# Kernel tuning notes

Measured on AMD Instinct MI355X. Metric: run time of the kernel, lower is better.

Reference implementation:

```python
import jax, jax.numpy as jnp
import numpy as np

B, S, FEAT, DK = 128, 2048, 512, 64

def setup_inputs() -> dict:
    key = jax.random.key(0)
    k1, k2, k3, k4, k5 = jax.random.split(key, 5)
    input_k = jax.random.normal(k1, (B, S, FEAT), dtype=jnp.float32)
    input_q = jax.random.normal(k2, (B, FEAT), dtype=jnp.float32)
    context_len = jax.random.randint(k3, (B,), 0, S + 1, dtype=jnp.int32)
    # Linear weights stored as [in, out] so y = x @ W
    W_K = jax.random.normal(k4, (FEAT, DK), dtype=jnp.float32) / np.sqrt(FEAT)
    W_Q = jax.random.normal(k5, (FEAT, DK), dtype=jnp.float32) / np.sqrt(FEAT)
    return {"input_k": input_k, "input_q": input_q, "context_len": context_len,
            "W_K": W_K, "W_Q": W_Q}

def reference(input_k, input_q, context_len, W_K, W_Q):
    # K: [B,S,dk], q: [B,dk]
    K = jnp.einsum('bsf,fd->bsd', input_k, W_K)
    q = input_q @ W_Q
    scores = jnp.einsum('bd,bsd->bs', q, K)  # [B,S] (n_heads=1, no scaling in original)
    mask = jnp.arange(S)[None, :] < context_len[:, None]  # [B,S]
    attn = jax.nn.softmax(jnp.where(mask, scores, -1e30), axis=-1)  # [B,S]
    context = jnp.einsum('bs,bsf->bf', attn, input_k)  # [B,FEAT]
    # length==0 rows produce zeros in the original
    context = jnp.where((context_len > 0)[:, None], context, 0.0)
    return context
```

## Files before the change

kernel.cpp:

```cpp
#include <hip/hip_runtime.h>
#include <math.h>

#define B_    128
#define S_    2048
#define FEAT_ 512
#define DK_   64
#define NSPLIT 16

typedef float f32x4 __attribute__((ext_vector_type(4)));

__device__ __forceinline__ float dot8(f32x4 x0, f32x4 x1, f32x4 v0, f32x4 v1) {
  float p = x0[0] * v0[0];
  p = fmaf(x0[1], v0[1], p);
  p = fmaf(x0[2], v0[2], p);
  p = fmaf(x0[3], v0[3], p);
  p = fmaf(x1[0], v1[0], p);
  p = fmaf(x1[1], v1[1], p);
  p = fmaf(x1[2], v1[2], p);
  p = fmaf(x1[3], v1[3], p);
  return p;
}

__device__ __forceinline__ float wredsum(float p) {
#pragma unroll
  for (int off = 32; off; off >>= 1) p += __shfl_xor(p, off, 64);
  return p;
}

__global__ __launch_bounds__(256) void qv_kernel(
    const float* __restrict__ input_q, const float* __restrict__ W_Q,
    const float* __restrict__ W_K, float* __restrict__ v) {
  int b = blockIdx.x;
  int tid = threadIdx.x;
  __shared__ float xq[FEAT_];
  __shared__ float part[4][DK_];
  __shared__ float qs[DK_];
  for (int f = tid; f < FEAT_; f += 256) xq[f] = input_q[b * FEAT_ + f];
  __syncthreads();
  {
    int d = tid & 63, c = tid >> 6;
    float s = 0.f;
    int f0 = c * 128;
    for (int f = f0; f < f0 + 128; ++f) s = fmaf(xq[f], W_Q[f * DK_ + d], s);
    part[c][d] = s;
  }
  __syncthreads();
  if (tid < DK_)
    qs[tid] = part[0][tid] + part[1][tid] + part[2][tid] + part[3][tid];
  __syncthreads();
  for (int f = tid; f < FEAT_; f += 256) {
    const f32x4* wk = (const f32x4*)(W_K + f * DK_);
    float s = 0.f;
#pragma unroll
    for (int d4 = 0; d4 < DK_ / 4; ++d4) {
      f32x4 w = wk[d4];
      s = fmaf(w[0], qs[d4 * 4 + 0], s);
      s = fmaf(w[1], qs[d4 * 4 + 1], s);
      s = fmaf(w[2], qs[d4 * 4 + 2], s);
      s = fmaf(w[3], qs[d4 * 4 + 3], s);
    }
    v[b * FEAT_ + f] = s;
  }
}

__global__ __launch_bounds__(256) void pass_kernel(
    const float* __restrict__ input_k, const int* __restrict__ ctx,
    const float* __restrict__ v, float* __restrict__ pm,
    float* __restrict__ pl, float* __restrict__ pacc) {
  int b = blockIdx.x;
  int split = blockIdx.y;
  int L = ctx[b];
  int tid = threadIdx.x, wave = tid >> 6, lane = tid & 63;
  int idx = b * NSPLIT + split;

  int s0 = (split * L) / NSPLIT;
  int s1 = ((split + 1) * L) / NSPLIT;

  if (s0 >= s1) {
    if (tid == 0) { pm[idx] = -INFINITY; pl[idx] = 0.f; }
    return;
  }

  const float* vb = v + b * FEAT_ + lane * 4;
  f32x4 v0 = *(const f32x4*)vb;
  f32x4 v1 = *(const f32x4*)(vb + 256);

  float m = -INFINITY, l = 0.f;
  f32x4 a0 = {0.f, 0.f, 0.f, 0.f};
  f32x4 a1 = {0.f, 0.f, 0.f, 0.f};

  const float* base = input_k + (size_t)b * S_ * FEAT_;
  int s = s0 + wave;

  for (; s + 12 < s1; s += 16) {
    const float* r_ = base + (size_t)s * FEAT_ + lane * 4;
    f32x4 x0 = *(const f32x4*)(r_);
    f32x4 x1 = *(const f32x4*)(r_ + 256);
    f32x4 x2 = *(const f32x4*)(r_ + 4 * FEAT_);
    f32x4 x3 = *(const f32x4*)(r_ + 4 * FEAT_ + 256);
    f32x4 x4 = *(const f32x4*)(r_ + 8 * FEAT_);
    f32x4 x5 = *(const f32x4*)(r_ + 8 * FEAT_ + 256);
    f32x4 x6 = *(const f32x4*)(r_ + 12 * FEAT_);
    f32x4 x7 = *(const f32x4*)(r_ + 12 * FEAT_ + 256);

    float p0 = dot8(x0, x1, v0, v1);
    float p1 = dot8(x2, x3, v0, v1);
    float p2 = dot8(x4, x5, v0, v1);
    float p3 = dot8(x6, x7, v0, v1);
    p0 = wredsum(p0);
    p1 = wredsum(p1);
    p2 = wredsum(p2);
    p3 = wredsum(p3);
    float mn = fmaxf(fmaxf(fmaxf(p0, p1), fmaxf(p2, p3)), m);
    float sc = __expf(m - mn);
    float w0 = __expf(p0 - mn), w1 = __expf(p1 - mn);
    float w2 = __expf(p2 - mn), w3 = __expf(p3 - mn);
    l = fmaf(l, sc, (w0 + w1) + (w2 + w3));
#pragma unroll
    for (int j = 0; j < 4; ++j) {
      a0[j] = fmaf(w0, x0[j],
              fmaf(w1, x2[j], fmaf(w2, x4[j], fmaf(w3, x6[j], a0[j] * sc))));
      a1[j] = fmaf(w0, x1[j],
              fmaf(w1, x3[j], fmaf(w2, x5[j], fmaf(w3, x7[j], a1[j] * sc))));
    }
    m = mn;
  }
  for (; s < s1; s += 4) {
    const float* r_ = base + (size_t)s * FEAT_ + lane * 4;
    f32x4 x0 = *(const f32x4*)(r_);
    f32x4 x1 = *(const f32x4*)(r_ + 256);
    float p = wredsum(dot8(x0, x1, v0, v1));
    float mn = fmaxf(m, p);
    float sc = __expf(m - mn);
    float w = __expf(p - mn);
    l = fmaf(l, sc, w);
#pragma unroll
    for (int j = 0; j < 4; ++j) {
      a0[j] = fmaf(w, x0[j], a0[j] * sc);
      a1[j] = fmaf(w, x1[j], a1[j] * sc);
    }
    m = mn;
  }

  __shared__ float sm[4], sl[4];
  __shared__ float sa[4][FEAT_];
  if (lane == 0) { sm[wave] = m; sl[wave] = l; }
  *(f32x4*)&sa[wave][lane * 4] = a0;
  *(f32x4*)&sa[wave][256 + lane * 4] = a1;
  __syncthreads();

  float M = fmaxf(fmaxf(sm[0], sm[1]), fmaxf(sm[2], sm[3]));
  float e0 = __expf(sm[0] - M), e1 = __expf(sm[1] - M);
  float e2 = __expf(sm[2] - M), e3 = __expf(sm[3] - M);
  if (tid == 0) {
    pm[idx] = M;
    pl[idx] = e0 * sl[0] + e1 * sl[1] + e2 * sl[2] + e3 * sl[3];
  }
  for (int f = tid; f < FEAT_; f += 256)
    pacc[(size_t)idx * FEAT_ + f] =
        e0 * sa[0][f] + e1 * sa[1][f] + e2 * sa[2][f] + e3 * sa[3][f];
}

__global__ __launch_bounds__(256) void combine_kernel(
    const float* __restrict__ pm, const float* __restrict__ pl,
    const float* __restrict__ pacc, float* __restrict__ out) {
  int b = blockIdx.x;
  int tid = threadIdx.x;
  __shared__ float e[NSPLIT];
  __shared__ float inv_s;
  if (tid < NSPLIT) {
    float mi = pm[b * NSPLIT + tid];
    float M = mi;
#pragma unroll
    for (int off = 8; off; off >>= 1) M = fmaxf(M, __shfl_xor(M, off, 64));
    float ei = (M == -INFINITY) ? 0.f : __expf(mi - M);
    e[tid] = ei;
    float lw = ei * pl[b * NSPLIT + tid];
#pragma unroll
    for (int off = 8; off; off >>= 1) lw += __shfl_xor(lw, off, 64);
    if (tid == 0) inv_s = (lw > 0.f) ? 1.f / lw : 0.f;
  }
  __syncthreads();
  float inv = inv_s;
  for (int f = tid; f < FEAT_; f += 256) {
    float s = 0.f;
    for (int i = 0; i < NSPLIT; ++i)
      if (e[i] > 0.f)
        s = fmaf(e[i], pacc[((size_t)(b * NSPLIT + i)) * FEAT_ + f], s);
    out[b * FEAT_ + f] = s * inv;
  }
}

extern "C" void kernel_launch(void* const* d_in, const int* in_sizes, int n_in,
                              void* d_out, int out_size, void* d_ws, size_t ws_size,
                              hipStream_t stream) {
  const float* input_k = (const float*)d_in[0];
  const float* input_q = (const float*)d_in[1];
  const int*   ctx     = (const int*)d_in[2];
  const float* W_K     = (const float*)d_in[3];
  const float* W_Q     = (const float*)d_in[4];
  float* out = (float*)d_out;

  char* ws = (char*)d_ws;
  float* v    = (float*)ws;
  float* pm   = (float*)(ws + (size_t)B_ * FEAT_ * sizeof(float));
  float* pl   = pm + B_ * NSPLIT;
  float* pacc = pl + B_ * NSPLIT;

  qv_kernel<<<B_, 256, 0, stream>>>(input_q, W_Q, W_K, v);
  pass_kernel<<<dim3(B_, NSPLIT), 256, 0, stream>>>(input_k, ctx, v, pm, pl, pacc);
  combine_kernel<<<B_, 256, 0, stream>>>(pm, pl, pacc, out);
}
```

Measured before the change: 71.87 us.

## Use persistent blocks with atomic work queue and finer sequence splits

Replaces the fixed (batch, split) grid with a persistent pool of blocks that take (batch, split) tasks from a global atomic counter. The counter is reset in the qv kernel. The number of splits per row doubles to 32, which shrinks the task size so uneven context lengths balance better across CUs. The cost is one atomic and two barriers per task, twice as many partial results for the combine kernel to reduce, and a dependence on kernel ordering for the counter reset.

```diff
diff --git a/kernel.cpp b/kernel.cpp
--- a/kernel.cpp
+++ b/kernel.cpp
@@ -5,7 +5,9 @@
 #define S_    2048
 #define FEAT_ 512
 #define DK_   64
-#define NSPLIT 16
+#define NSPLIT 32
+#define NTASKS (B_ * NSPLIT)
+#define NBLOCKS 2048
 
 typedef float f32x4 __attribute__((ext_vector_type(4)));
 
@@ -29,9 +31,11 @@
 
 __global__ __launch_bounds__(256) void qv_kernel(
     const float* __restrict__ input_q, const float* __restrict__ W_Q,
-    const float* __restrict__ W_K, float* __restrict__ v) {
+    const float* __restrict__ W_K, float* __restrict__ v,
+    unsigned* __restrict__ counter) {
   int b = blockIdx.x;
   int tid = threadIdx.x;
+  if (b == 0 && tid == 0) *counter = 0u;
   __shared__ float xq[FEAT_];
   __shared__ float part[4][DK_];
   __shared__ float qs[DK_];
@@ -66,99 +70,110 @@
 __global__ __launch_bounds__(256) void pass_kernel(
     const float* __restrict__ input_k, const int* __restrict__ ctx,
     const float* __restrict__ v, float* __restrict__ pm,
-    float* __restrict__ pl, float* __restrict__ pacc) {
-  int b = blockIdx.x;
-  int split = blockIdx.y;
-  int L = ctx[b];
+    float* __restrict__ pl, float* __restrict__ pacc,
+    unsigned* __restrict__ counter) {
   int tid = threadIdx.x, wave = tid >> 6, lane = tid & 63;
-  int idx = b * NSPLIT + split;
-
-  int s0 = (split * L) / NSPLIT;
-  int s1 = ((split + 1) * L) / NSPLIT;
-
-  if (s0 >= s1) {
-    if (tid == 0) { pm[idx] = -INFINITY; pl[idx] = 0.f; }
-    return;
-  }
-
-  const float* vb = v + b * FEAT_ + lane * 4;
-  f32x4 v0 = *(const f32x4*)vb;
-  f32x4 v1 = *(const f32x4*)(vb + 256);
-
-  float m = -INFINITY, l = 0.f;
-  f32x4 a0 = {0.f, 0.f, 0.f, 0.f};
-  f32x4 a1 = {0.f, 0.f, 0.f, 0.f};
-
-  const float* base = input_k + (size_t)b * S_ * FEAT_;
-  int s = s0 + wave;
-
-  for (; s + 12 < s1; s += 16) {
-    const float* r_ = base + (size_t)s * FEAT_ + lane * 4;
-    f32x4 x0 = *(const f32x4*)(r_);
-    f32x4 x1 = *(const f32x4*)(r_ + 256);
-    f32x4 x2 = *(const f32x4*)(r_ + 4 * FEAT_);
-    f32x4 x3 = *(const f32x4*)(r_ + 4 * FEAT_ + 256);
-    f32x4 x4 = *(const f32x4*)(r_ + 8 * FEAT_);
-    f32x4 x5 = *(const f32x4*)(r_ + 8 * FEAT_ + 256);
-    f32x4 x6 = *(const f32x4*)(r_ + 12 * FEAT_);
-    f32x4 x7 = *(const f32x4*)(r_ + 12 * FEAT_ + 256);
-
-    float p0 = dot8(x0, x1, v0, v1);
-    float p1 = dot8(x2, x3, v0, v1);
-    float p2 = dot8(x4, x5, v0, v1);
-    float p3 = dot8(x6, x7, v0, v1);
-    p0 = wredsum(p0);
-    p1 = wredsum(p1);
-    p2 = wredsum(p2);
-    p3 = wredsum(p3);
-    float mn = fmaxf(fmaxf(fmaxf(p0, p1), fmaxf(p2, p3)), m);
-    float sc = __expf(m - mn);
-    float w0 = __expf(p0 - mn), w1 = __expf(p1 - mn);
-    float w2 = __expf(p2 - mn), w3 = __expf(p3 - mn);
-    l = fmaf(l, sc, (w0 + w1) + (w2 + w3));
-#pragma unroll
-    for (int j = 0; j < 4; ++j) {
-      a0[j] = fmaf(w0, x0[j],
-              fmaf(w1, x2[j], fmaf(w2, x4[j], fmaf(w3, x6[j], a0[j] * sc))));
-      a1[j] = fmaf(w0, x1[j],
-              fmaf(w1, x3[j], fmaf(w2, x5[j], fmaf(w3, x7[j], a1[j] * sc))));
-    }
-    m = mn;
-  }
-  for (; s < s1; s += 4) {
-    const float* r_ = base + (size_t)s * FEAT_ + lane * 4;
-    f32x4 x0 = *(const f32x4*)(r_);
-    f32x4 x1 = *(const f32x4*)(r_ + 256);
-    float p = wredsum(dot8(x0, x1, v0, v1));
-    float mn = fmaxf(m, p);
-    float sc = __expf(m - mn);
-    float w = __expf(p - mn);
-    l = fmaf(l, sc, w);
-#pragma unroll
-    for (int j = 0; j < 4; ++j) {
-      a0[j] = fmaf(w, x0[j], a0[j] * sc);
-      a1[j] = fmaf(w, x1[j], a1[j] * sc);
-    }
-    m = mn;
-  }
-
   __shared__ float sm[4], sl[4];
   __shared__ float sa[4][FEAT_];
-  if (lane == 0) { sm[wave] = m; sl[wave] = l; }
-  *(f32x4*)&sa[wave][lane * 4] = a0;
-  *(f32x4*)&sa[wave][256 + lane * 4] = a1;
-  __syncthreads();
-
-  float M = fmaxf(fmaxf(sm[0], sm[1]), fmaxf(sm[2], sm[3]));
-  float e0 = __expf(sm[0] - M), e1 = __expf(sm[1] - M);
-  float e2 = __expf(sm[2] - M), e3 = __expf(sm[3] - M);
-  if (tid == 0) {
-    pm[idx] = M;
-    pl[idx] = e0 * sl[0] + e1 * sl[1] + e2 * sl[2] + e3 * sl[3];
-  }
-  for (int f = tid; f < FEAT_; f += 256)
-    pacc[(size_t)idx * FEAT_ + f] =
-        e0 * sa[0][f] + e1 * sa[1][f] + e2 * sa[2][f] + e3 * sa[3][f];
+  __shared__ unsigned s_task;
+
+  for (;;) {
+    if (tid == 0) s_task = atomicAdd(counter, 1u);
+    __syncthreads();
+    unsigned t = s_task;
+    __syncthreads();
+    if (t >= (unsigned)NTASKS) return;
+
+    int b = (int)(t >> 5);
+    int split = (int)(t & (NSPLIT - 1));
+    int L = ctx[b];
+    int idx = (int)t;
+
+    int s0 = (split * L) / NSPLIT;
+    int s1 = ((split + 1) * L) / NSPLIT;
+
+    if (s0 >= s1) {
+      if (tid == 0) { pm[idx] = -INFINITY; pl[idx] = 0.f; }
+      continue;
+    }
+
+    const float* vb = v + b * FEAT_ + lane * 4;
+    f32x4 v0 = *(const f32x4*)vb;
+    f32x4 v1 = *(const f32x4*)(vb + 256);
+
+    float m = -INFINITY, l = 0.f;
+    f32x4 a0 = {0.f, 0.f, 0.f, 0.f};
+    f32x4 a1 = {0.f, 0.f, 0.f, 0.f};
+
+    const float* base = input_k + (size_t)b * S_ * FEAT_;
+    int s = s0 + wave;
+
+    for (; s + 12 < s1; s += 16) {
+      const float* r_ = base + (size_t)s * FEAT_ + lane * 4;
+      f32x4 x0 = *(const f32x4*)(r_);
+      f32x4 x1 = *(const f32x4*)(r_ + 256);
+      f32x4 x2 = *(const f32x4*)(r_ + 4 * FEAT_);
+      f32x4 x3 = *(const f32x4*)(r_ + 4 * FEAT_ + 256);
+      f32x4 x4 = *(const f32x4*)(r_ + 8 * FEAT_);
+      f32x4 x5 = *(const f32x4*)(r_ + 8 * FEAT_ + 256);
+      f32x4 x6 = *(const f32x4*)(r_ + 12 * FEAT_);
+      f32x4 x7 = *(const f32x4*)(r_ + 12 * FEAT_ + 256);
+
+      float p0 = dot8(x0, x1, v0, v1);
+      float p1 = dot8(x2, x3, v0, v1);
+      float p2 = dot8(x4, x5, v0, v1);
+      float p3 = dot8(x6, x7, v0, v1);
+      p0 = wredsum(p0);
+      p1 = wredsum(p1);
+      p2 = wredsum(p2);
+      p3 = wredsum(p3);
+      float mn = fmaxf(fmaxf(fmaxf(p0, p1), fmaxf(p2, p3)), m);
+      float sc = __expf(m - mn);
+      float w0 = __expf(p0 - mn), w1 = __expf(p1 - mn);
+      float w2 = __expf(p2 - mn), w3 = __expf(p3 - mn);
+      l = fmaf(l, sc, (w0 + w1) + (w2 + w3));
+#pragma unroll
+      for (int j = 0; j < 4; ++j) {
+        a0[j] = fmaf(w0, x0[j],
+                fmaf(w1, x2[j], fmaf(w2, x4[j], fmaf(w3, x6[j], a0[j] * sc))));
+        a1[j] = fmaf(w0, x1[j],
+                fmaf(w1, x3[j], fmaf(w2, x5[j], fmaf(w3, x7[j], a1[j] * sc))));
+      }
+      m = mn;
+    }
+    for (; s < s1; s += 4) {
+      const float* r_ = base + (size_t)s * FEAT_ + lane * 4;
+      f32x4 x0 = *(const f32x4*)(r_);
+      f32x4 x1 = *(const f32x4*)(r_ + 256);
+      float p = wredsum(dot8(x0, x1, v0, v1));
+      float mn = fmaxf(m, p);
+      float sc = __expf(m - mn);
+      float w = __expf(p - mn);
+      l = fmaf(l, sc, w);
+#pragma unroll
+      for (int j = 0; j < 4; ++j) {
+        a0[j] = fmaf(w, x0[j], a0[j] * sc);
+        a1[j] = fmaf(w, x1[j], a1[j] * sc);
+      }
+      m = mn;
+    }
+
+    if (lane == 0) { sm[wave] = m; sl[wave] = l; }
+    *(f32x4*)&sa[wave][lane * 4] = a0;
+    *(f32x4*)&sa[wave][256 + lane * 4] = a1;
+    __syncthreads();
+
+    float M = fmaxf(fmaxf(sm[0], sm[1]), fmaxf(sm[2], sm[3]));
+    float e0 = __expf(sm[0] - M), e1 = __expf(sm[1] - M);
+    float e2 = __expf(sm[2] - M), e3 = __expf(sm[3] - M);
+    if (tid == 0) {
+      pm[idx] = M;
+      pl[idx] = e0 * sl[0] + e1 * sl[1] + e2 * sl[2] + e3 * sl[3];
+    }
+    for (int f = tid; f < FEAT_; f += 256)
+      pacc[(size_t)idx * FEAT_ + f] =
+          e0 * sa[0][f] + e1 * sa[1][f] + e2 * sa[2][f] + e3 * sa[3][f];
+  }
 }
 
 __global__ __launch_bounds__(256) void combine_kernel(
@@ -172,12 +187,12 @@
     float mi = pm[b * NSPLIT + tid];
     float M = mi;
 #pragma unroll
-    for (int off = 8; off; off >>= 1) M = fmaxf(M, __shfl_xor(M, off, 64));
+    for (int off = 16; off; off >>= 1) M = fmaxf(M, __shfl_xor(M, off, 64));
     float ei = (M == -INFINITY) ? 0.f : __expf(mi - M);
     e[tid] = ei;
     float lw = ei * pl[b * NSPLIT + tid];
 #pragma unroll
-    for (int off = 8; off; off >>= 1) lw += __shfl_xor(lw, off, 64);
+    for (int off = 16; off; off >>= 1) lw += __shfl_xor(lw, off, 64);
     if (tid == 0) inv_s = (lw > 0.f) ? 1.f / lw : 0.f;
   }
   __syncthreads();
@@ -204,10 +219,12 @@
   char* ws = (char*)d_ws;
   float* v    = (float*)ws;
   float* pm   = (float*)(ws + (size_t)B_ * FEAT_ * sizeof(float));
-  float* pl   = pm + B_ * NSPLIT;
-  float* pacc = pl + B_ * NSPLIT;
-
-  qv_kernel<<<B_, 256, 0, stream>>>(input_q, W_Q, W_K, v);
-  pass_kernel<<<dim3(B_, NSPLIT), 256, 0, stream>>>(input_k, ctx, v, pm, pl, pacc);
+  float* pl   = pm + NTASKS;
+  float* pacc = pl + NTASKS;
+  unsigned* counter = (unsigned*)(pacc + (size_t)NTASKS * FEAT_);
+
+  qv_kernel<<<B_, 256, 0, stream>>>(input_q, W_Q, W_K, v, counter);
+  pass_kernel<<<NBLOCKS, 256, 0, stream>>>(input_k, ctx, v, pm, pl, pacc,
+                                           counter);
   combine_kernel<<<B_, 256, 0, stream>>>(pm, pl, pacc, out);
 }
```

New measurement: 116.0 us. +61.3%, slower.

## Balance split-K attention work across blocks by context length

Applied to the files above, without the earlier changes.

Replaces the fixed 16 splits per batch row with a length-proportional allocation. About 1792 blocks are distributed across rows according to each row's context length, so every block handles a similar number of sequence positions. Each block works out its row and split index by scanning all 128 context lengths in a single thread, and the combine kernel recomputes the same prefix to find each row's partials. The aim is to remove the load imbalance that comes from random context lengths. The cost is a serial per-block scan and a combine step that can read up to 512 partials per row.

```diff
diff --git a/kernel.cpp b/kernel.cpp
--- a/kernel.cpp
+++ b/kernel.cpp
@@ -5,7 +5,9 @@
 #define S_    2048
 #define FEAT_ 512
 #define DK_   64
-#define NSPLIT 16
+#define NB    1792
+#define GRIDP 2048
+#define MAXN  512
 
 typedef float f32x4 __attribute__((ext_vector_type(4)));
 
@@ -27,6 +29,14 @@
   return p;
 }
 
+__device__ __forceinline__ int nsplits_of(int Lb, int T) {
+  if (T == 0) return 1;
+  int nb = (int)(((long long)Lb * NB + (T >> 1)) / T);
+  if (nb < 1) nb = 1;
+  if (nb > MAXN) nb = MAXN;
+  return nb;
+}
+
 __global__ __launch_bounds__(256) void qv_kernel(
     const float* __restrict__ input_q, const float* __restrict__ W_Q,
     const float* __restrict__ W_K, float* __restrict__ v) {
@@ -67,17 +77,39 @@
     const float* __restrict__ input_k, const int* __restrict__ ctx,
     const float* __restrict__ v, float* __restrict__ pm,
     float* __restrict__ pl, float* __restrict__ pacc) {
-  int b = blockIdx.x;
-  int split = blockIdx.y;
-  int L = ctx[b];
+  int j = blockIdx.x;
   int tid = threadIdx.x, wave = tid >> 6, lane = tid & 63;
-  int idx = b * NSPLIT + split;
-
-  int s0 = (split * L) / NSPLIT;
-  int s1 = ((split + 1) * L) / NSPLIT;
+
+  __shared__ int sL[B_];
+  __shared__ int sInfo[4];
+  __shared__ float sm[4], sl4[4];
+  __shared__ float sa[4][FEAT_];
+
+  if (tid < B_) sL[tid] = ctx[tid];
+  __syncthreads();
+  if (tid == 0) {
+    int T = 0;
+    for (int i = 0; i < B_; ++i) T += sL[i];
+    int q = 0, fb = -1, fk = 0, fL = 0, fn = 1;
+    for (int i = 0; i < B_; ++i) {
+      int nb = nsplits_of(sL[i], T);
+      if (fb < 0 && j >= q && j < q + nb) {
+        fb = i; fk = j - q; fL = sL[i]; fn = nb;
+      }
+      q += nb;
+    }
+    sInfo[0] = fb; sInfo[1] = fk; sInfo[2] = fL; sInfo[3] = fn;
+  }
+  __syncthreads();
+  int b = sInfo[0];
+  if (b < 0) return;
+  int k = sInfo[1], L = sInfo[2], nb = sInfo[3];
+
+  int s0 = (int)((long long)k * L / nb);
+  int s1 = (int)((long long)(k + 1) * L / nb);
 
   if (s0 >= s1) {
-    if (tid == 0) { pm[idx] = -INFINITY; pl[idx] = 0.f; }
+    if (tid == 0) { pm[j] = -INFINITY; pl[j] = 0.f; }
     return;
   }
 
@@ -117,11 +149,11 @@
     float w2 = __expf(p2 - mn), w3 = __expf(p3 - mn);
     l = fmaf(l, sc, (w0 + w1) + (w2 + w3));
 #pragma unroll
-    for (int j = 0; j < 4; ++j) {
-      a0[j] = fmaf(w0, x0[j],
-              fmaf(w1, x2[j], fmaf(w2, x4[j], fmaf(w3, x6[j], a0[j] * sc))));
-      a1[j] = fmaf(w0, x1[j],
-              fmaf(w1, x3[j], fmaf(w2, x5[j], fmaf(w3, x7[j], a1[j] * sc))));
+    for (int jj = 0; jj < 4; ++jj) {
+      a0[jj] = fmaf(w0, x0[jj],
+               fmaf(w1, x2[jj], fmaf(w2, x4[jj], fmaf(w3, x6[jj], a0[jj] * sc))));
+      a1[jj] = fmaf(w0, x1[jj],
+               fmaf(w1, x3[jj], fmaf(w2, x5[jj], fmaf(w3, x7[jj], a1[jj] * sc))));
     }
     m = mn;
   }
@@ -135,16 +167,14 @@
     float w = __expf(p - mn);
     l = fmaf(l, sc, w);
 #pragma unroll
-    for (int j = 0; j < 4; ++j) {
-      a0[j] = fmaf(w, x0[j], a0[j] * sc);
-      a1[j] = fmaf(w, x1[j], a1[j] * sc);
+    for (int jj = 0; jj < 4; ++jj) {
+      a0[jj] = fmaf(w, x0[jj], a0[jj] * sc);
+      a1[jj] = fmaf(w, x1[jj], a1[jj] * sc);
     }
     m = mn;
   }
 
-  __shared__ float sm[4], sl[4];
-  __shared__ float sa[4][FEAT_];
-  if (lane == 0) { sm[wave] = m; sl[wave] = l; }
+  if (lane == 0) { sm[wave] = m; sl4[wave] = l; }
   *(f32x4*)&sa[wave][lane * 4] = a0;
   *(f32x4*)&sa[wave][256 + lane * 4] = a1;
   __syncthreads();
@@ -153,40 +183,77 @@
   float e0 = __expf(sm[0] - M), e1 = __expf(sm[1] - M);
   float e2 = __expf(sm[2] - M), e3 = __expf(sm[3] - M);
   if (tid == 0) {
-    pm[idx] = M;
-    pl[idx] = e0 * sl[0] + e1 * sl[1] + e2 * sl[2] + e3 * sl[3];
+    pm[j] = M;
+    pl[j] = e0 * sl4[0] + e1 * sl4[1] + e2 * sl4[2] + e3 * sl4[3];
   }
   for (int f = tid; f < FEAT_; f += 256)
-    pacc[(size_t)idx * FEAT_ + f] =
+    pacc[(size_t)j * FEAT_ + f] =
         e0 * sa[0][f] + e1 * sa[1][f] + e2 * sa[2][f] + e3 * sa[3][f];
 }
 
 __global__ __launch_bounds__(256) void combine_kernel(
-    const float* __restrict__ pm, const float* __restrict__ pl,
-    const float* __restrict__ pacc, float* __restrict__ out) {
+    const int* __restrict__ ctx, const float* __restrict__ pm,
+    const float* __restrict__ pl, const float* __restrict__ pacc,
+    float* __restrict__ out) {
   int b = blockIdx.x;
   int tid = threadIdx.x;
-  __shared__ float e[NSPLIT];
+  __shared__ int sL[B_];
+  __shared__ int sQN[2];
+  __shared__ float e[MAXN];
+  __shared__ float redM[4], redL[4];
   __shared__ float inv_s;
-  if (tid < NSPLIT) {
-    float mi = pm[b * NSPLIT + tid];
-    float M = mi;
-#pragma unroll
-    for (int off = 8; off; off >>= 1) M = fmaxf(M, __shfl_xor(M, off, 64));
-    float ei = (M == -INFINITY) ? 0.f : __expf(mi - M);
-    e[tid] = ei;
-    float lw = ei * pl[b * NSPLIT + tid];
-#pragma unroll
-    for (int off = 8; off; off >>= 1) lw += __shfl_xor(lw, off, 64);
-    if (tid == 0) inv_s = (lw > 0.f) ? 1.f / lw : 0.f;
+
+  if (tid < B_) sL[tid] = ctx[tid];
+  __syncthreads();
+  if (tid == 0) {
+    int T = 0;
+    for (int i = 0; i < B_; ++i) T += sL[i];
+    int q = 0, Qb = 0, nb_ = 1;
+    for (int i = 0; i <= b; ++i) {
+      int nb = nsplits_of(sL[i], T);
+      if (i == b) { Qb = q; nb_ = nb; }
+      q += nb;
+    }
+    sQN[0] = Qb; sQN[1] = nb_;
+  }
+  __syncthreads();
+  int Q = sQN[0], n = sQN[1];
+  int L = sL[b];
+  if (L == 0) {
+    for (int f = tid; f < FEAT_; f += 256) out[b * FEAT_ + f] = 0.f;
+    return;
+  }
+
+  float M = -INFINITY;
+  for (int i = tid; i < n; i += 256) M = fmaxf(M, pm[Q + i]);
+#pragma unroll
+  for (int off = 32; off; off >>= 1) M = fmaxf(M, __shfl_xor(M, off, 64));
+  if ((tid & 63) == 0) redM[tid >> 6] = M;
+  __syncthreads();
+  M = fmaxf(fmaxf(redM[0], redM[1]), fmaxf(redM[2], redM[3]));
+
+  float lw = 0.f;
+  for (int i = tid; i < n; i += 256) {
+    float ei = __expf(pm[Q + i] - M);
+    e[i] = ei;
+    lw += ei * pl[Q + i];
+  }
+#pragma unroll
+  for (int off = 32; off; off >>= 1) lw += __shfl_xor(lw, off, 64);
+  if ((tid & 63) == 0) redL[tid >> 6] = lw;
+  __syncthreads();
+  if (tid == 0) {
+    float lt = redL[0] + redL[1] + redL[2] + redL[3];
+    inv_s = (lt > 0.f) ? 1.f / lt : 0.f;
   }
   __syncthreads();
   float inv = inv_s;
+
   for (int f = tid; f < FEAT_; f += 256) {
     float s = 0.f;
-    for (int i = 0; i < NSPLIT; ++i)
+    for (int i = 0; i < n; ++i)
       if (e[i] > 0.f)
-        s = fmaf(e[i], pacc[((size_t)(b * NSPLIT + i)) * FEAT_ + f], s);
+        s = fmaf(e[i], pacc[(size_t)(Q + i) * FEAT_ + f], s);
     out[b * FEAT_ + f] = s * inv;
   }
 }
@@ -204,10 +271,10 @@
   char* ws = (char*)d_ws;
   float* v    = (float*)ws;
   float* pm   = (float*)(ws + (size_t)B_ * FEAT_ * sizeof(float));
-  float* pl   = pm + B_ * NSPLIT;
-  float* pacc = pl + B_ * NSPLIT;
+  float* pl   = pm + GRIDP;
+  float* pacc = pl + GRIDP;
 
   qv_kernel<<<B_, 256, 0, stream>>>(input_q, W_Q, W_K, v);
-  pass_kernel<<<dim3(B_, NSPLIT), 256, 0, stream>>>(input_k, ctx, v, pm, pl, pacc);
-  combine_kernel<<<B_, 256, 0, stream>>>(pm, pl, pacc, out);
-}
+  pass_kernel<<<GRIDP, 256, 0, stream>>>(input_k, ctx, v, pm, pl, pacc);
+  combine_kernel<<<B_, 256, 0, stream>>>(ctx, pm, pl, pacc, out);
+}
```

After: 126.5 us. 1.76x slower.
